# Optimization experiments

Hardware: AMD Instinct MI355X
Metric: run time of the kernel (lower is better)

The kernel has to match this reference:

```python
import math
import jax, jax.numpy as jnp
import numpy as np

B, T, D, CHUNK = 16, 8192, 128, 64


def setup_inputs() -> dict:
    key = jax.random.key(0)
    kq, kk, kv = jax.random.split(key, 3)
    q = jax.random.normal(kq, (B, T, D), dtype=jnp.float32)
    k = jax.random.normal(kk, (B, T, D), dtype=jnp.float32)
    v = jax.random.normal(kv, (B, T, D), dtype=jnp.float32)
    # learnable per-head decay parameter, init so sigmoid(log_decay) = 0.99
    log_decay = jnp.full((1,), math.log(0.99 / (1.0 - 0.99)), dtype=jnp.float32)
    return {"q": q, "k": k, "v": v, "log_decay": log_decay, "chunk_size": CHUNK}


def reference(q, k, v, log_decay, chunk_size):
    """Chunk-wise parallel forward of DecayedLinearState.parallel_forward.

    Returns (output [B,T,D], final_state [B,D,D], final_z [B,D]).
    """
    lam = jax.nn.sigmoid(log_decay[0])
    Bb, Tt, Dd = q.shape
    C = int(chunk_size)
    pad = (-Tt) % C
    if pad:
        q = jnp.pad(q, ((0, 0), (0, pad), (0, 0)))
        k = jnp.pad(k, ((0, 0), (0, pad), (0, 0)))
        v = jnp.pad(v, ((0, 0), (0, pad), (0, 0)))
    N = (Tt + pad) // C
    qc = q.reshape(Bb, N, C, D)  # [B,N,C,D]
    kc = k.reshape(Bb, N, C, D)
    vc = v.reshape(Bb, N, C, D)

    pos = jnp.arange(C, dtype=q.dtype)
    rel = pos[:, None] - pos[None, :]                      # i - j
    causal = jnp.tril(jnp.ones((C, C), dtype=q.dtype))
    decay_matrix = (lam ** jnp.maximum(rel, 0.0)) * causal  # [C,C]

    # intra-chunk attention for all chunks in parallel
    attn = jnp.einsum('bnic,bnjc->bnij', qc, kc) * decay_matrix  # [B,N,C,C]
    intra_out = jnp.einsum('bnij,bnjd->bnid', attn, vc)          # [B,N,C,D]
    intra_z = jnp.maximum(attn.sum(-1), 1.0)                     # [B,N,C]

    decay_q = lam ** (pos + 1.0)           # decay applied to cross-chunk reads [C]
    chunk_decay = lam ** (C - 1.0 - pos)   # decay applied to state writes     [C]
    state_decay = lam ** C

    weighted_outer = jnp.einsum('bnci,bncj,c->bnij', kc, vc, chunk_decay)  # [B,N,D,D]
    k_sum = jnp.einsum('bnci,c->bni', kc, chunk_decay)                     # [B,N,D]

    def step(carry, xs):
        state, z = carry  # [B,D,D], [B,D]
        qcn, io_n, iz_n, wo_n, ks_n = xs
        cross_out = jnp.einsum('bij,bci->bcj', state, qcn) * decay_q[None, :, None]
        cross_z = jnp.einsum('bi,bci->bc', z, qcn) * decay_q[None, :]
        total_z = jnp.maximum(iz_n + cross_z, 1.0)[..., None]
        out = (io_n + cross_out) / total_z                     # [B,C,D]
        new_state = state_decay * state + wo_n
        new_z = state_decay * z + ks_n
        return (new_state, new_z), out

    init = (jnp.zeros((Bb, D, D), q.dtype), jnp.zeros((Bb, D), q.dtype))
    xs = (qc.transpose(1, 0, 2, 3), intra_out.transpose(1, 0, 2, 3),
          intra_z.transpose(1, 0, 2), weighted_outer.transpose(1, 0, 2, 3),
          k_sum.transpose(1, 0, 2))
    (state, z), outs = jax.lax.scan(step, init, xs)  # outs: [N,B,C,D]
    output = outs.transpose(1, 0, 2, 3).reshape(Bb, N * C, D)[:, :Tt]
    return output, state, z
```

## Files before the change

kernel.cpp:

```cpp
#include <hip/hip_runtime.h>
#include <math.h>

#define Bn  16
#define Tn  8192
#define Dn  128
#define Cn  64
#define Gn  8
#define NGn 16
#define GCn 512

typedef __attribute__((ext_vector_type(8)))  short short8v;
typedef __attribute__((ext_vector_type(16))) float f32x16;

#define AK  200
#define BK  200
#define KDs 136
#define KTs 72
#define KFs 132
#define K1s 72

#define SWZ(row) ((((row) >> 2) & 7) << 3)

#define BAR() do { asm volatile("s_waitcnt lgkmcnt(0)" ::: "memory"); \
                   __builtin_amdgcn_s_barrier(); \
                   asm volatile("" ::: "memory"); } while (0)

__device__ __forceinline__ float sig_(float x){ return 1.0f/(1.0f+expf(-x)); }

__device__ __forceinline__ unsigned short f2bf(float f){
    __bf16 h = (__bf16)f;
    return __builtin_bit_cast(unsigned short, h);
}
__device__ __forceinline__ void st4(unsigned short* p, float a, float b, float c, float d){
    ushort4 u; u.x = f2bf(a); u.y = f2bf(b); u.z = f2bf(c); u.w = f2bf(d);
    *(ushort4*)p = u;
}

template<int CTRL>
__device__ __forceinline__ float dppadd(float x){
    int y = __builtin_amdgcn_update_dpp(0, __builtin_bit_cast(int, x), CTRL, 0xf, 0xf, true);
    return x + __builtin_bit_cast(float, y);
}
__device__ __forceinline__ float red32(float x){
    x = dppadd<0xB1>(x);
    x = dppadd<0x4E>(x);
    x = dppadd<0x124>(x);
    x = dppadd<0x128>(x);
    x = dppadd<0x142>(x);
    return x;
}

__global__ __launch_bounds__(512)
void k1_mfma(const float* __restrict__ kin, const float* __restrict__ vin,
             const float* __restrict__ log_decay,
             float* __restrict__ A, float* __restrict__ ksumg)
{
    const int g = blockIdx.x, b = blockIdx.y;
    const int tid  = threadIdx.x;
    const int wid  = tid >> 6;
    const int lane = tid & 63;
    const int l31  = lane & 31;
    const int lhi  = lane >> 5;
    const float lam = sig_(log_decay[0]);

    __shared__ __align__(16) unsigned short kT[128*K1s];
    __shared__ __align__(16) unsigned short vT[128*K1s];
    __shared__ float wt[GCn];
    __shared__ __align__(16) float ps[16*132];

    wt[tid] = powf(lam, (float)(GCn-1 - tid));

    const size_t base = ((size_t)b*Tn + (size_t)g*GCn)*Dn;
    const int rb = tid >> 5;
    const int cb = (tid & 31)*4;

    f32x16 acc[2];
    #pragma unroll
    for (int p = 0; p < 2; ++p)
        #pragma unroll
        for (int r = 0; r < 16; ++r) acc[p][r] = 0.f;
    float ksp[4] = {0.f, 0.f, 0.f, 0.f};

    float kv[4][4], vv[4][4];
    {
        const float* kp = kin + base;
        const float* vp = vin + base;
        #pragma unroll
        for (int u = 0; u < 4; ++u) {
            float4 t4 = *(const float4*)&kp[(size_t)(rb*4+u)*Dn + cb];
            kv[u][0]=t4.x; kv[u][1]=t4.y; kv[u][2]=t4.z; kv[u][3]=t4.w;
            float4 s4 = *(const float4*)&vp[(size_t)(rb*4+u)*Dn + cb];
            vv[u][0]=s4.x; vv[u][1]=s4.y; vv[u][2]=s4.z; vv[u][3]=s4.w;
        }
    }
    BAR();

    const int tr0 = (wid >> 2)*2;
    const int tc  = (wid & 3)*32;

    for (int t = 0; t < 8; ++t) {
        const int r0 = rb*4;
        float w0 = wt[t*64 + r0+0], w1 = wt[t*64 + r0+1];
        float w2 = wt[t*64 + r0+2], w3 = wt[t*64 + r0+3];
        #pragma unroll
        for (int e = 0; e < 4; ++e) {
            int row = cb+e, col = r0 ^ SWZ(row);
            float a0 = kv[0][e]*w0, a1 = kv[1][e]*w1, a2 = kv[2][e]*w2, a3 = kv[3][e]*w3;
            ksp[e] += (a0 + a1) + (a2 + a3);
            st4(&kT[row*K1s + col], a0, a1, a2, a3);
            st4(&vT[row*K1s + col], vv[0][e], vv[1][e], vv[2][e], vv[3][e]);
        }
        BAR();

        if (t < 7) {
            const float* kp = kin + base + (size_t)(t+1)*64*Dn;
            const float* vp = vin + base + (size_t)(t+1)*64*Dn;
            #pragma unroll
            for (int u = 0; u < 4; ++u) {
                float4 t4 = *(const float4*)&kp[(size_t)(rb*4+u)*Dn + cb];
                kv[u][0]=t4.x; kv[u][1]=t4.y; kv[u][2]=t4.z; kv[u][3]=t4.w;
                float4 s4 = *(const float4*)&vp[(size_t)(rb*4+u)*Dn + cb];
                vv[u][0]=s4.x; vv[u][1]=s4.y; vv[u][2]=s4.z; vv[u][3]=s4.w;
            }
        }

        #pragma unroll
        for (int kk = 0; kk < 4; ++kk) {
            int rB = tc + l31;
            short8v bf = *(const short8v*)&vT[rB*K1s + ((kk*16 + lhi*8) ^ SWZ(rB))];
            #pragma unroll
            for (int p = 0; p < 2; ++p) {
                int rA = (tr0+p)*32 + l31;
                short8v af = *(const short8v*)&kT[rA*K1s + ((kk*16 + lhi*8) ^ SWZ(rA))];
                acc[p] = __builtin_amdgcn_mfma_f32_32x32x16_bf16(af, bf, acc[p], 0, 0, 0);
            }
        }
        BAR();
    }

    float* Ab = A + ((size_t)(b*NGn + g))*Dn*Dn;
    #pragma unroll
    for (int p = 0; p < 2; ++p) {
        #pragma unroll
        for (int r = 0; r < 16; ++r) {
            int i = (tr0+p)*32 + (r&3) + 8*(r>>2) + 4*lhi;
            Ab[(size_t)i*Dn + tc + l31] = acc[p][r];
        }
    }

    *(float4*)&ps[rb*132 + cb] = make_float4(ksp[0], ksp[1], ksp[2], ksp[3]);
    BAR();
    if (tid < Dn) {
        float s = 0.f;
        #pragma unroll
        for (int q = 0; q < 16; ++q) s += ps[q*132 + tid];
        ksumg[((size_t)(b*NGn+g))*Dn + tid] = s;
    }
}

__global__ __launch_bounds__(256)
void k2_scan(const float* __restrict__ A, const float* __restrict__ ksumg,
             const float* __restrict__ log_decay,
             float* __restrict__ Sg, float* __restrict__ zg,
             float* __restrict__ outState, float* __restrict__ outZ)
{
    const int idx = blockIdx.x*256 + threadIdx.x;
    const float lam = sig_(log_decay[0]);
    const float dG = powf(lam, (float)GCn);
    const int NSTATE = Bn*Dn*Dn;
    if (idx < NSTATE) {
        const int b = idx >> 14, ij = idx & 16383;
        float s = 0.f;
        #pragma unroll
        for (int g = 0; g < NGn; ++g) {
            size_t o = (((size_t)(b*NGn+g)) << 14) + ij;
            Sg[o] = s;
            s = dG*s + A[o];
        }
        outState[idx] = s;
    } else if (idx < NSTATE + Bn*Dn) {
        const int j = idx - NSTATE, b = j >> 7, d = j & 127;
        float s = 0.f;
        #pragma unroll
        for (int g = 0; g < NGn; ++g) {
            size_t o = (size_t)(b*NGn+g)*Dn + d;
            zg[o] = s;
            s = dG*s + ksumg[o];
        }
        outZ[j] = s;
    }
}

__global__ __launch_bounds__(512, 2)
void k3_mfma(const float* __restrict__ qin, const float* __restrict__ kin,
             const float* __restrict__ vin, const float* __restrict__ log_decay,
             const float* __restrict__ Sg, const float* __restrict__ zg,
             float* __restrict__ out)
{
    const int g = blockIdx.x, b = blockIdx.y;
    const int tid  = threadIdx.x;
    const int wid  = tid >> 6;
    const int lane = tid & 63;
    const int l31  = lane & 31;
    const int lhi  = lane >> 5;
    const float lam   = sig_(log_decay[0]);
    const float lam64 = powf(lam, 64.0f);

    __shared__ __align__(16) unsigned short sA [64*AK];
    __shared__ __align__(16) unsigned short sB [128*BK];
    __shared__ __align__(16) unsigned short sKd[64*KDs];
    __shared__ __align__(16) unsigned short sKT[128*KTs];
    __shared__ __align__(16) float kf[64*KFs];
    __shared__ __align__(16) float zf[128];
    __shared__ __align__(16) float izb[64], czb[64];
    __shared__ float ptabs[66], ntabs[64];

    const int bg = b*NGn + g;
    const size_t base = (size_t)b*Tn + (size_t)g*Gn*Cn;

    if (tid < 66)  ptabs[tid] = powf(lam, (float)tid);
    if (tid >= 66 && tid < 130) ntabs[tid-66] = powf(lam, -(float)(tid-65));
    if (tid < 128) zf[tid] = zg[(size_t)bg*Dn + tid];

    f32x16 sacc[4];
    if (wid >= 4) {
        const float* Sgp = Sg + ((size_t)bg << 14);
        const int er0 = (wid-4)*32;
        #pragma unroll
        for (int ct = 0; ct < 4; ++ct) {
            const int d = ct*32 + l31;
            #pragma unroll
            for (int r = 0; r < 16; ++r) {
                int e = er0 + (r&3) + 8*(r>>2) + 4*lhi;
                sacc[ct][r] = Sgp[e*Dn + d];
            }
            #pragma unroll
            for (int q = 0; q < 4; ++q) {
                int e0 = er0 + 8*q + 4*lhi;
                st4(&sB[d*BK + 64 + e0],
                    sacc[ct][4*q], sacc[ct][4*q+1], sacc[ct][4*q+2], sacc[ct][4*q+3]);
            }
        }
    }

    const int a4  = (tid >> 5)*4;
    const int b4c = (tid & 31)*4;

    float qv[4][4], kv[4][4], vv[4][4];
    #pragma unroll
    for (int u = 0; u < 4; ++u) {
        float4 tq = *(const float4*)&qin[(base + a4+u)*Dn + b4c];
        qv[u][0]=tq.x; qv[u][1]=tq.y; qv[u][2]=tq.z; qv[u][3]=tq.w;
        float4 tk = *(const float4*)&kin[(base + a4+u)*Dn + b4c];
        kv[u][0]=tk.x; kv[u][1]=tk.y; kv[u][2]=tk.z; kv[u][3]=tk.w;
        float4 tv = *(const float4*)&vin[(base + a4+u)*Dn + b4c];
        vv[u][0]=tv.x; vv[u][1]=tv.y; vv[u][2]=tv.z; vv[u][3]=tv.w;
    }

    const int r0 = (wid >> 2)*32;
    const int c0 = (wid & 3)*32;

    BAR();

    for (int m = 0; m < Gn; ++m) {
        const size_t rowbase = base + (size_t)m*Cn;

        float qc[4][4];
        #pragma unroll
        for (int u = 0; u < 4; ++u) {
            const int row = a4 + u;
            const float s = ptabs[row+1];
            st4(&sA[row*AK + 64 + b4c], qv[u][0]*s, qv[u][1]*s, qv[u][2]*s, qv[u][3]*s);
            #pragma unroll
            for (int x = 0; x < 4; ++x) qc[u][x] = qv[u][x];
        }
        #pragma unroll
        for (int u = 0; u < 4; ++u)
            *(float4*)&kf[(a4+u)*KFs + b4c] = make_float4(kv[u][0],kv[u][1],kv[u][2],kv[u][3]);
        #pragma unroll
        for (int u = 0; u < 4; ++u) {
            float s = ntabs[a4+u];
            st4(&sKd[(a4+u)*KDs + b4c], kv[u][0]*s, kv[u][1]*s, kv[u][2]*s, kv[u][3]*s);
        }
        {
            float w0 = ptabs[63-a4], w1 = ptabs[62-a4], w2 = ptabs[61-a4], w3 = ptabs[60-a4];
            #pragma unroll
            for (int e = 0; e < 4; ++e) {
                int row = b4c + e, col = a4 ^ SWZ(row);
                st4(&sKT[row*KTs + col], kv[0][e]*w0, kv[1][e]*w1, kv[2][e]*w2, kv[3][e]*w3);
                st4(&sB [row*BK  + col], vv[0][e], vv[1][e], vv[2][e], vv[3][e]);
            }
        }
        if (m + 1 < Gn) {
            const size_t nrow = rowbase + Cn;
            #pragma unroll
            for (int u = 0; u < 4; ++u) {
                float4 tq = *(const float4*)&qin[(nrow + a4+u)*Dn + b4c];
                qv[u][0]=tq.x; qv[u][1]=tq.y; qv[u][2]=tq.z; qv[u][3]=tq.w;
                float4 tk = *(const float4*)&kin[(nrow + a4+u)*Dn + b4c];
                kv[u][0]=tk.x; kv[u][1]=tk.y; kv[u][2]=tk.z; kv[u][3]=tk.w;
                float4 tv = *(const float4*)&vin[(nrow + a4+u)*Dn + b4c];
                vv[u][0]=tv.x; vv[u][1]=tv.y; vv[u][2]=tv.z; vv[u][3]=tv.w;
            }
        }
        BAR();

        if (wid < 2) {
            const int d = tid;
            float kap = 0.f;
            for (int bb = 0; bb < 4; ++bb) {
                float rr[16];
                #pragma unroll
                for (int j = 0; j < 16; ++j) rr[j] = kf[(bb*16+j)*KFs + d];
                #pragma unroll
                for (int j = 0; j < 16; ++j) { kap = lam*kap + rr[j]; rr[j] = kap; }
                #pragma unroll
                for (int j = 0; j < 16; ++j) kf[(bb*16+j)*KFs + d] = rr[j];
            }
        } else if (wid < 4) {
            const int ic = (wid - 2)*32;
            #pragma unroll
            for (int jj = 0; jj < 2; ++jj) {
                const int jr = jj*32;
                f32x16 acc;
                #pragma unroll
                for (int r = 0; r < 16; ++r) acc[r] = 0.f;
                #pragma unroll
                for (int kk = 0; kk < 8; ++kk) {
                    short8v af = *(const short8v*)&sKd[(jr + l31)*KDs + kk*16 + lhi*8];
                    short8v bf = *(const short8v*)&sA [(ic + l31)*AK + 64 + kk*16 + lhi*8];
                    acc = __builtin_amdgcn_mfma_f32_32x32x16_bf16(af, bf, acc, 0, 0, 0);
                }
                const int i = ic + l31;
                #pragma unroll
                for (int q = 0; q < 4; ++q) {
                    int j0 = jr + 8*q + 4*lhi;
                    float v0 = (j0+0 <= i) ? acc[4*q+0] : 0.f;
                    float v1 = (j0+1 <= i) ? acc[4*q+1] : 0.f;
                    float v2 = (j0+2 <= i) ? acc[4*q+2] : 0.f;
                    float v3 = (j0+3 <= i) ? acc[4*q+3] : 0.f;
                    st4(&sA[i*AK + j0], v0, v1, v2, v3);
                }
            }
        } else {
            const int er0 = (wid-4)*32;
            #pragma unroll
            for (int ct = 0; ct < 4; ++ct)
                #pragma unroll
                for (int r = 0; r < 16; ++r) sacc[ct][r] *= lam64;
            #pragma unroll
            for (int kk = 0; kk < 4; ++kk) {
                int rA = er0 + l31;
                short8v af = *(const short8v*)&sKT[rA*KTs + ((kk*16 + lhi*8) ^ SWZ(rA))];
                #pragma unroll
                for (int ct = 0; ct < 4; ++ct) {
                    int rB = ct*32 + l31;
                    short8v bf = *(const short8v*)&sB[rB*BK + ((kk*16 + lhi*8) ^ SWZ(rB))];
                    sacc[ct] = __builtin_amdgcn_mfma_f32_32x32x16_bf16(af, bf, sacc[ct], 0, 0, 0);
                }
            }
        }
        BAR();

        {
            float aI[4], aZ[4];
            float4 zv = *(const float4*)&zf[b4c];
            #pragma unroll
            for (int u = 0; u < 4; ++u) {
                float4 kp = *(const float4*)&kf[(a4+u)*KFs + b4c];
                aI[u] = qc[u][0]*kp.x + qc[u][1]*kp.y + qc[u][2]*kp.z + qc[u][3]*kp.w;
                aZ[u] = qc[u][0]*zv.x + qc[u][1]*zv.y + qc[u][2]*zv.z + qc[u][3]*zv.w;
            }
            #pragma unroll
            for (int u = 0; u < 4; ++u) { aI[u] = red32(aI[u]); aZ[u] = red32(aZ[u]); }
            if ((lane & 31) == 16) {
                #pragma unroll
                for (int u = 0; u < 4; ++u) {
                    izb[a4+u] = aI[u];
                    czb[a4+u] = ptabs[a4+u+1]*aZ[u];
                }
            }
        }
        f32x16 oacc;
        #pragma unroll
        for (int r = 0; r < 16; ++r) oacc[r] = 0.f;
        #pragma unroll
        for (int kk = 0; kk < 12; ++kk) {
            short8v af = *(const short8v*)&sA[(r0 + l31)*AK + kk*16 + lhi*8];
            int rB = c0 + l31;
            int coff = kk*16 + lhi*8;
            if (kk < 4) coff ^= SWZ(rB);
            short8v bf = *(const short8v*)&sB[rB*BK + coff];
            oacc = __builtin_amdgcn_mfma_f32_32x32x16_bf16(af, bf, oacc, 0, 0, 0);
        }
        BAR();

        #pragma unroll
        for (int r = 0; r < 16; ++r) {
            int t = r0 + (r&3) + 8*(r>>2) + 4*lhi;
            float tz = fmaxf(fmaxf(izb[t], 1.f) + czb[t], 1.f);
            out[(rowbase + t)*Dn + c0 + l31] = oacc[r] * __builtin_amdgcn_rcpf(tz);
        }
        if (wid >= 4) {
            const int er0 = (wid-4)*32;
            #pragma unroll
            for (int ct = 0; ct < 4; ++ct) {
                const int d = ct*32 + l31;
                #pragma unroll
                for (int q = 0; q < 4; ++q) {
                    int e0 = er0 + 8*q + 4*lhi;
                    st4(&sB[d*BK + 64 + e0],
                        sacc[ct][4*q], sacc[ct][4*q+1], sacc[ct][4*q+2], sacc[ct][4*q+3]);
                }
            }
        }
        if (tid < 128) {
            zf[tid] = lam64*zf[tid] + kf[63*KFs + tid];
        }
        BAR();
    }
}

extern "C" void kernel_launch(void* const* d_in, const int* in_sizes, int n_in,
                              void* d_out, int out_size, void* d_ws, size_t ws_size,
                              hipStream_t stream)
{
    const float* q  = (const float*)d_in[0];
    const float* k  = (const float*)d_in[1];
    const float* v  = (const float*)d_in[2];
    const float* ld = (const float*)d_in[3];
    float* out = (float*)d_out;

    float* A     = (float*)d_ws;
    float* ksumg = A     + (size_t)Bn*NGn*Dn*Dn;
    float* Sg    = ksumg + (size_t)Bn*NGn*Dn;
    float* zg    = Sg    + (size_t)Bn*NGn*Dn*Dn;

    float* outState = out      + (size_t)Bn*Tn*Dn;
    float* outZ     = outState + (size_t)Bn*Dn*Dn;

    hipLaunchKernelGGL(k1_mfma, dim3(NGn, Bn), dim3(512), 0, stream,
                       k, v, ld, A, ksumg);

    const int total2 = Bn*Dn*Dn + Bn*Dn;
    hipLaunchKernelGGL(k2_scan, dim3((total2 + 255)/256), dim3(256), 0, stream,
                       A, ksumg, ld, Sg, zg, outState, outZ);

    hipLaunchKernelGGL(k3_mfma, dim3(NGn, Bn), dim3(512), 0, stream,
                       q, k, v, ld, Sg, zg, out);
}
```

Before: 87.40 us.

## Software-pipeline chunk loop: defer output stores, split MFMA phases, double-buffer z

Restructures the per-chunk loop so the output normalization/store and the state write-back into shared memory for chunk m happen at the start of iteration m+1. This removes one barrier per iteration. The cross-chunk MFMA (k-steps 4..11) now runs before the first barrier, and the intra-chunk part (k-steps 0..3) runs after it. The z vector is double-buffered so its update no longer needs its own barrier, and s_setprio is raised around the MFMA blocks. The reordering depends on subtle shared-memory hazards (sB state columns, izb/czb reuse across iterations), which add correctness risk.

```diff
diff --git a/kernel.cpp b/kernel.cpp
--- a/kernel.cpp
+++ b/kernel.cpp
@@ -211,7 +211,7 @@
     __shared__ __align__(16) unsigned short sKd[64*KDs];
     __shared__ __align__(16) unsigned short sKT[128*KTs];
     __shared__ __align__(16) float kf[64*KFs];
-    __shared__ __align__(16) float zf[128];
+    __shared__ __align__(16) float zf[2*128];
     __shared__ __align__(16) float izb[64], czb[64];
     __shared__ float ptabs[66], ntabs[64];
 
@@ -259,12 +259,33 @@
 
     const int r0 = (wid >> 2)*32;
     const int c0 = (wid & 3)*32;
-
-    BAR();
+    f32x16 oacc;
 
     for (int m = 0; m < Gn; ++m) {
         const size_t rowbase = base + (size_t)m*Cn;
 
+        if (m > 0) {
+            const size_t prow = rowbase - Cn;
+            #pragma unroll
+            for (int r = 0; r < 16; ++r) {
+                int t = r0 + (r&3) + 8*(r>>2) + 4*lhi;
+                float tz = fmaxf(fmaxf(izb[t], 1.f) + czb[t], 1.f);
+                out[(prow + t)*Dn + c0 + l31] = oacc[r] * __builtin_amdgcn_rcpf(tz);
+            }
+            if (wid >= 4) {
+                const int er0 = (wid-4)*32;
+                #pragma unroll
+                for (int ct = 0; ct < 4; ++ct) {
+                    const int d = ct*32 + l31;
+                    #pragma unroll
+                    for (int q = 0; q < 4; ++q) {
+                        int e0 = er0 + 8*q + 4*lhi;
+                        st4(&sB[d*BK + 64 + e0],
+                            sacc[ct][4*q], sacc[ct][4*q+1], sacc[ct][4*q+2], sacc[ct][4*q+3]);
+                    }
+                }
+            }
+        }
         float qc[4][4];
         #pragma unroll
         for (int u = 0; u < 4; ++u) {
@@ -348,6 +369,7 @@
             for (int ct = 0; ct < 4; ++ct)
                 #pragma unroll
                 for (int r = 0; r < 16; ++r) sacc[ct][r] *= lam64;
+            __builtin_amdgcn_s_setprio(1);
             #pragma unroll
             for (int kk = 0; kk < 4; ++kk) {
                 int rA = er0 + l31;
@@ -359,12 +381,23 @@
                     sacc[ct] = __builtin_amdgcn_mfma_f32_32x32x16_bf16(af, bf, sacc[ct], 0, 0, 0);
                 }
             }
-        }
+            __builtin_amdgcn_s_setprio(0);
+        }
+        #pragma unroll
+        for (int r = 0; r < 16; ++r) oacc[r] = 0.f;
+        __builtin_amdgcn_s_setprio(1);
+        #pragma unroll
+        for (int kk = 4; kk < 12; ++kk) {
+            short8v af = *(const short8v*)&sA[(r0 + l31)*AK + kk*16 + lhi*8];
+            short8v bf = *(const short8v*)&sB[(c0 + l31)*BK + kk*16 + lhi*8];
+            oacc = __builtin_amdgcn_mfma_f32_32x32x16_bf16(af, bf, oacc, 0, 0, 0);
+        }
+        __builtin_amdgcn_s_setprio(0);
         BAR();
 
         {
             float aI[4], aZ[4];
-            float4 zv = *(const float4*)&zf[b4c];
+            float4 zv = *(const float4*)&zf[(m & 1)*128 + b4c];
             #pragma unroll
             for (int u = 0; u < 4; ++u) {
                 float4 kp = *(const float4*)&kf[(a4+u)*KFs + b4c];
@@ -381,43 +414,29 @@
                 }
             }
         }
-        f32x16 oacc;
-        #pragma unroll
-        for (int r = 0; r < 16; ++r) oacc[r] = 0.f;
-        #pragma unroll
-        for (int kk = 0; kk < 12; ++kk) {
+        if (tid < 128) {
+            zf[((m+1)&1)*128 + tid] = lam64*zf[(m&1)*128 + tid] + kf[63*KFs + tid];
+        }
+        __builtin_amdgcn_s_setprio(1);
+        #pragma unroll
+        for (int kk = 0; kk < 4; ++kk) {
             short8v af = *(const short8v*)&sA[(r0 + l31)*AK + kk*16 + lhi*8];
             int rB = c0 + l31;
-            int coff = kk*16 + lhi*8;
-            if (kk < 4) coff ^= SWZ(rB);
-            short8v bf = *(const short8v*)&sB[rB*BK + coff];
+            short8v bf = *(const short8v*)&sB[rB*BK + ((kk*16 + lhi*8) ^ SWZ(rB))];
             oacc = __builtin_amdgcn_mfma_f32_32x32x16_bf16(af, bf, oacc, 0, 0, 0);
         }
+        __builtin_amdgcn_s_setprio(0);
         BAR();
-
+    }
+
+    {
+        const size_t prow = base + (size_t)(Gn-1)*Cn;
         #pragma unroll
         for (int r = 0; r < 16; ++r) {
             int t = r0 + (r&3) + 8*(r>>2) + 4*lhi;
             float tz = fmaxf(fmaxf(izb[t], 1.f) + czb[t], 1.f);
-            out[(rowbase + t)*Dn + c0 + l31] = oacc[r] * __builtin_amdgcn_rcpf(tz);
-        }
-        if (wid >= 4) {
-            const int er0 = (wid-4)*32;
-            #pragma unroll
-            for (int ct = 0; ct < 4; ++ct) {
-                const int d = ct*32 + l31;
-                #pragma unroll
-                for (int q = 0; q < 4; ++q) {
-                    int e0 = er0 + 8*q + 4*lhi;
-                    st4(&sB[d*BK + 64 + e0],
-                        sacc[ct][4*q], sacc[ct][4*q+1], sacc[ct][4*q+2], sacc[ct][4*q+3]);
-                }
-            }
-        }
-        if (tid < 128) {
-            zf[tid] = lam64*zf[tid] + kf[63*KFs + tid];
-        }
-        BAR();
+            out[(prow + t)*Dn + c0 + l31] = oacc[r] * __builtin_amdgcn_rcpf(tz);
+        }
     }
 }
 
```

After: 106.4 us. 21.7% more time.
